# Kernel optimization log

Measured on AMD Instinct MI355X. Metric: run time of the kernel, lower is better.

The kernel has to match this reference:

```python
import jax, jax.numpy as jnp
import numpy as np

N = 50000   # nodes
E = 800000  # edges (avg degree 16)
IN, H, OUT = 128, 128, 128


def _lin(key, fan_in, fan_out):
    s = 1.0 / np.sqrt(fan_in)
    return jax.random.uniform(key, (fan_in, fan_out), minval=-s, maxval=s, dtype=jnp.float32)


def setup_inputs() -> dict:
    key = jax.random.key(0)
    ks = jax.random.split(key, 12)
    inp = {
        "x": jax.random.normal(ks[0], (N, IN), dtype=jnp.float32),
        "edge_index": jax.random.randint(ks[1], (2, E), 0, N, dtype=jnp.int64),
        # layer 1: in -> hidden
        "Wl1": _lin(ks[2], IN, H), "b1": jnp.zeros((H,), jnp.float32), "Wr1": _lin(ks[3], IN, H),
        # layer 2: hidden -> hidden
        "Wl2": _lin(ks[4], H, H), "b2": jnp.zeros((H,), jnp.float32), "Wr2": _lin(ks[5], H, H),
        # layer 3: hidden -> out
        "Wl3": _lin(ks[6], H, OUT), "b3": jnp.zeros((OUT,), jnp.float32), "Wr3": _lin(ks[7], H, OUT),
    }
    return inp


def _sage_conv(x, src, dst, inv_deg, Wl, b, Wr):
    # mean-aggregate neighbor messages: gather from src, scatter-sum to dst
    msg = jnp.take(x, src, axis=0)                       # [E, d]
    agg = jax.ops.segment_sum(msg, dst, num_segments=N)  # [N, d]
    mean = agg * inv_deg[:, None]                        # scatter-mean (0 for isolated)
    return mean @ Wl + b + x @ Wr


def reference(x, edge_index, Wl1, b1, Wr1, Wl2, b2, Wr2, Wl3, b3, Wr3):
    src, dst = edge_index[0], edge_index[1]
    deg = jax.ops.segment_sum(jnp.ones((E,), jnp.float32), dst, num_segments=N)
    inv_deg = jnp.where(deg > 0, 1.0 / jnp.maximum(deg, 1.0), 0.0)

    h = _sage_conv(x, src, dst, inv_deg, Wl1, b1, Wr1)
    h = jax.nn.relu(h)  # dropout p=0.5 is identity in eval mode
    h = _sage_conv(h, src, dst, inv_deg, Wl2, b2, Wr2)
    h = jax.nn.relu(h)
    h = _sage_conv(h, src, dst, inv_deg, Wl3, b3, Wr3)
    return h
```

## Files before the change

kernel.cpp:

```cpp
#include <hip/hip_runtime.h>


#define D 128

typedef __attribute__((ext_vector_type(8))) short bf16x8;
typedef __attribute__((ext_vector_type(4))) float f32x4;

__device__ inline ushort f2bf(float f) {
  union { float f; unsigned u; } v; v.f = f;
  unsigned r = v.u + 0x7fffu + ((v.u >> 16) & 1u);
  return (ushort)(r >> 16);
}
__device__ inline float bf2f(ushort h) {
  union { unsigned u; float f; } v; v.u = ((unsigned)h) << 16;
  return v.f;
}

__global__ __launch_bounds__(256) void k_bhist(const int* __restrict__ dst,
                                               int* __restrict__ bhist, int E, int NB) {
  __shared__ int h[512];
  int t = threadIdx.x;
  for (int i = t; i < NB; i += 256) h[i] = 0;
  __syncthreads();
  int beg = blockIdx.x * 4096;
  int end = min(beg + 4096, E);
  for (int i = beg + t; i < end; i += 256) atomicAdd(&h[dst[i] >> 7], 1);
  __syncthreads();
  for (int i = t; i < NB; i += 256)
    if (h[i]) atomicAdd(&bhist[i], h[i]);
}

__global__ __launch_bounds__(512) void k_bscan(const int* __restrict__ bhist,
                                               int* __restrict__ bbase,
                                               int* __restrict__ bcur,
                                               int* __restrict__ offN, int NB) {
  __shared__ int part[512];
  int t = threadIdx.x;
  part[t] = (t < NB) ? bhist[t] : 0;
  __syncthreads();
  for (int d = 1; d < 512; d <<= 1) {
    int x = part[t];
    int a = (t >= d) ? part[t - d] : 0;
    __syncthreads();
    part[t] = x + a;
    __syncthreads();
  }
  if (t < NB) {
    int b = (t == 0) ? 0 : part[t - 1];
    bbase[t] = b;
    bcur[t] = b;
  }
  if (t == NB - 1) *offN = part[t];
}

__global__ __launch_bounds__(256) void k_bucket(const int* __restrict__ src,
                                                const int* __restrict__ dst,
                                                int* __restrict__ bcur,
                                                unsigned* __restrict__ ebuf,
                                                int E, int NB) {
  __shared__ int h[512];
  __shared__ int base[512];
  int t = threadIdx.x;
  for (int i = t; i < NB; i += 256) h[i] = 0;
  __syncthreads();
  int beg = blockIdx.x * 4096;
  int end = min(beg + 4096, E);
  for (int i = beg + t; i < end; i += 256) atomicAdd(&h[dst[i] >> 7], 1);
  __syncthreads();
  for (int i = t; i < NB; i += 256) {
    int c = h[i];
    base[i] = c ? atomicAdd(&bcur[i], c) : 0;
    h[i] = 0;
  }
  __syncthreads();
  for (int i = beg + t; i < end; i += 256) {
    int d = dst[i];
    int b = d >> 7;
    int r = atomicAdd(&h[b], 1);
    ebuf[base[b] + r] = (((unsigned)src[i]) << 16) | (unsigned)d;
  }
}

__global__ __launch_bounds__(256) void k_csr(const unsigned* __restrict__ ebuf,
                                             const int* __restrict__ bbase,
                                             const int* __restrict__ bhist,
                                             int* __restrict__ off,
                                             float* __restrict__ invd,
                                             int* __restrict__ srcs, int N) {
  __shared__ int dcount[128];
  __shared__ int dloc[128];
  int b = blockIdx.x;
  int t = threadIdx.x;
  int beg = bbase[b];
  int end = beg + bhist[b];
  if (t < 128) dcount[t] = 0;
  __syncthreads();
  for (int i = beg + t; i < end; i += 256) atomicAdd(&dcount[ebuf[i] & 127], 1);
  __syncthreads();
  if (t < 128) dloc[t] = dcount[t];
  __syncthreads();
  for (int d = 1; d < 128; d <<= 1) {
    int x = 0, a = 0;
    if (t < 128) {
      x = dloc[t];
      if (t >= d) a = dloc[t - d];
    }
    __syncthreads();
    if (t < 128) dloc[t] = x + a;
    __syncthreads();
  }
  if (t < 128) {
    int node = b * 128 + t;
    if (node < N) {
      int ex = beg + dloc[t] - dcount[t];
      off[node] = ex;
      int c = dcount[t];
      invd[node] = c > 0 ? 1.0f / (float)c : 0.0f;
      dcount[t] = ex;
    }
  }
  __syncthreads();
  for (int i = beg + t; i < end; i += 256) {
    unsigned p = ebuf[i];
    int slot = atomicAdd(&dcount[p & 127], 1);
    srcs[slot] = (int)(p >> 16);
  }
}

__global__ void k_cast(const float* __restrict__ x, ushort* __restrict__ xb, int total4) {
  int i = blockIdx.x * blockDim.x + threadIdx.x;
  if (i >= total4) return;
  float4 v = *reinterpret_cast<const float4*>(x + (size_t)i * 4);
  ushort4 o;
  o.x = f2bf(v.x); o.y = f2bf(v.y); o.z = f2bf(v.z); o.w = f2bf(v.w);
  *reinterpret_cast<ushort4*>(xb + (size_t)i * 4) = o;
}

__global__ void k_pack3(const float* __restrict__ Wl1, const float* __restrict__ Wr1,
                        const float* __restrict__ Wl2, const float* __restrict__ Wr2,
                        const float* __restrict__ Wl3, const float* __restrict__ Wr3,
                        ushort* __restrict__ Bp) {
  int gidx = blockIdx.x * blockDim.x + threadIdx.x;
  int layer = gidx >> 15;
  int idx = gidx & 32767;
  const float* Wl = (layer == 0) ? Wl1 : (layer == 1) ? Wl2 : Wl3;
  const float* Wr = (layer == 0) ? Wr1 : (layer == 1) ? Wr2 : Wr3;
  int kk = idx >> 12;
  int ct = (idx >> 9) & 7;
  int l  = (idx >> 3) & 63;
  int j  = idx & 7;
  int k = kk * 32 + ((l >> 4) << 3) + j;
  int col = ct * 16 + (l & 15);
  float v = (k < 128) ? Wl[k * 128 + col] : Wr[(k - 128) * 128 + col];
  Bp[gidx] = f2bf(v);
}

template <int RELU, int FINAL>
__global__ __launch_bounds__(256, 6) void k_fused(const ushort* __restrict__ hin,
                                                  const int* __restrict__ off,
                                                  const int* __restrict__ srcs,
                                                  const float* __restrict__ invd,
                                                  const ushort* __restrict__ Bpack,
                                                  const float* __restrict__ bias,
                                                  float* __restrict__ outf,
                                                  ushort* __restrict__ outh, int N) {
  __shared__ ushort smean[16 * D];
  int t = threadIdx.x;
  int w = t >> 6;
  int lane = t & 63;
  int node0 = blockIdx.x * 16;
  int g = lane >> 4;
  int s = lane & 15;

  for (int q = 0; q < 4; ++q) {
    int nl = w * 4 + q;
    int n = node0 + nl;
    float acc[8] = {0.f, 0.f, 0.f, 0.f, 0.f, 0.f, 0.f, 0.f};
    float wgt = 0.f;
    if (n < N) {
      wgt = invd[n];
      int lo = off[n], hi = off[n + 1];
      int e = lo + g;
      for (; e + 4 < hi; e += 8) {
        int i0 = srcs[e];
        int i1 = srcs[e + 4];
        bf16x8 v0 = *reinterpret_cast<const bf16x8*>(hin + (size_t)i0 * D + s * 8);
        bf16x8 v1 = *reinterpret_cast<const bf16x8*>(hin + (size_t)i1 * D + s * 8);
#pragma unroll
        for (int j = 0; j < 8; ++j) acc[j] += bf2f((ushort)v0[j]);
#pragma unroll
        for (int j = 0; j < 8; ++j) acc[j] += bf2f((ushort)v1[j]);
      }
      if (e < hi) {
        int i0 = srcs[e];
        bf16x8 v0 = *reinterpret_cast<const bf16x8*>(hin + (size_t)i0 * D + s * 8);
#pragma unroll
        for (int j = 0; j < 8; ++j) acc[j] += bf2f((ushort)v0[j]);
      }
    }
#pragma unroll
    for (int j = 0; j < 8; ++j) acc[j] += __shfl_xor(acc[j], 16);
#pragma unroll
    for (int j = 0; j < 8; ++j) acc[j] += __shfl_xor(acc[j], 32);
    if (lane < 16) {
      bf16x8 o;
#pragma unroll
      for (int j = 0; j < 8; ++j) o[j] = (short)f2bf(acc[j] * wgt);
      int byte = nl * 256 + ((s * 16) ^ ((nl & 7) << 4));
      *reinterpret_cast<bf16x8*>(reinterpret_cast<char*>(smean) + byte) = o;
    }
  }
  __syncthreads();

  int lr = lane & 15;
  int kgrp = lane >> 4;
  int arow = node0 + lr;
  if (arow >= N) arow = N - 1;
  size_t abase = (size_t)arow * D;

  f32x4 acc2[2];
#pragma unroll
  for (int i = 0; i < 2; ++i) {
    float bv = bias[(w * 2 + i) * 16 + lr];
    acc2[i] = (f32x4){bv, bv, bv, bv};
  }

#pragma unroll
  for (int kk = 0; kk < 8; ++kk) {
    int klocal = ((kk & 3) << 5) + (kgrp << 3);
    bf16x8 a;
    if (kk < 4) {
      int byte = lr * 256 + ((klocal * 2) ^ ((lr & 7) << 4));
      a = *reinterpret_cast<const bf16x8*>(reinterpret_cast<const char*>(smean) + byte);
    } else {
      a = *reinterpret_cast<const bf16x8*>(hin + abase + klocal);
    }
#pragma unroll
    for (int i = 0; i < 2; ++i) {
      int ct = w * 2 + i;
      bf16x8 b = *reinterpret_cast<const bf16x8*>(Bpack + (((size_t)(kk * 8 + ct) * 64 + lane) << 3));
      acc2[i] = __builtin_amdgcn_mfma_f32_16x16x32_bf16(a, b, acc2[i], 0, 0, 0);
    }
  }

#pragma unroll
  for (int i = 0; i < 2; ++i) {
    int c = (w * 2 + i) * 16 + lr;
#pragma unroll
    for (int r = 0; r < 4; ++r) {
      int rr = node0 + kgrp * 4 + r;
      if (rr < N) {
        float v = acc2[i][r];
        if (RELU) v = fmaxf(v, 0.f);
        if (FINAL) outf[(size_t)rr * D + c] = v;
        else outh[(size_t)rr * D + c] = f2bf(v);
      }
    }
  }
}

extern "C" void kernel_launch(void* const* d_in, const int* in_sizes, int n_in,
                              void* d_out, int out_size, void* d_ws, size_t ws_size,
                              hipStream_t stream) {
  const float* x   = (const float*)d_in[0];
  const int*   ei  = (const int*)d_in[1];
  const float* Wl1 = (const float*)d_in[2];
  const float* b1  = (const float*)d_in[3];
  const float* Wr1 = (const float*)d_in[4];
  const float* Wl2 = (const float*)d_in[5];
  const float* b2  = (const float*)d_in[6];
  const float* Wr2 = (const float*)d_in[7];
  const float* Wl3 = (const float*)d_in[8];
  const float* b3  = (const float*)d_in[9];
  const float* Wr3 = (const float*)d_in[10];
  float* out = (float*)d_out;

  int N = in_sizes[0] / D;
  int E = in_sizes[1] / 2;
  const int* srcp = ei;
  const int* dstp = ei + E;
  int NB = (N + 127) >> 7;

  char* p = (char*)d_ws;
  auto carve = [&](size_t bytes) {
    void* r = (void*)p;
    p += (bytes + 255) & ~(size_t)255;
    return r;
  };
  int*      bhist = (int*)carve((size_t)512 * 4);
  int*      bbase = (int*)carve((size_t)512 * 4);
  int*      bcur  = (int*)carve((size_t)512 * 4);
  int*      off   = (int*)carve((size_t)(N + 1) * 4);
  float*    invd  = (float*)carve((size_t)N * 4);
  int*      srcs  = (int*)carve((size_t)E * 4);
  unsigned* ebuf  = (unsigned*)carve((size_t)E * 4);
  ushort*   xb    = (ushort*)carve((size_t)N * D * 2);
  ushort*   h1b   = (ushort*)carve((size_t)N * D * 2);
  ushort*   h2b   = (ushort*)carve((size_t)N * D * 2);
  ushort*   Bp    = (ushort*)carve((size_t)3 * 32768 * 2);

  hipMemsetAsync(bhist, 0, (size_t)NB * 4, stream);
  int ch_blocks = (E + 4095) / 4096;
  k_bhist<<<ch_blocks, 256, 0, stream>>>(dstp, bhist, E, NB);
  k_bscan<<<1, 512, 0, stream>>>(bhist, bbase, bcur, off + N, NB);
  k_bucket<<<ch_blocks, 256, 0, stream>>>(srcp, dstp, bcur, ebuf, E, NB);
  k_csr<<<NB, 256, 0, stream>>>(ebuf, bbase, bhist, off, invd, srcs, N);

  int total4 = N * D / 4;
  k_cast<<<(total4 + 255) / 256, 256, 0, stream>>>(x, xb, total4);
  k_pack3<<<3 * 32768 / 256, 256, 0, stream>>>(Wl1, Wr1, Wl2, Wr2, Wl3, Wr3, Bp);

  int fused_blocks = (N + 15) / 16;

  k_fused<1, 0><<<fused_blocks, 256, 0, stream>>>(xb, off, srcs, invd, Bp, b1, nullptr, h1b, N);
  k_fused<1, 0><<<fused_blocks, 256, 0, stream>>>(h1b, off, srcs, invd, Bp + 32768, b2, nullptr, h2b, N);
  k_fused<0, 1><<<fused_blocks, 256, 0, stream>>>(h2b, off, srcs, invd, Bp + 2 * 32768, b3, out, nullptr, N);
}
```

Measured before the change: 180.6 us.

## Fold bucket scan into histogram kernel and interleave two-node gathers

Removes the separate single-block scan launch: the last histogram block, found with an atomic counter in an unused slot of bhist (index 480), does a wavefront shuffle scan. The aggregation loop in the fused SAGE kernel now processes two nodes at once, issuing four independent row gathers per iteration so more memory loads are in flight. This trades one kernel launch and gather latency for higher register pressure and a dependence on NB staying below 480.

```diff
diff --git a/kernel.cpp b/kernel.cpp
--- a/kernel.cpp
+++ b/kernel.cpp
@@ -17,8 +17,13 @@
 }
 
 __global__ __launch_bounds__(256) void k_bhist(const int* __restrict__ dst,
-                                               int* __restrict__ bhist, int E, int NB) {
+                                               int* __restrict__ bhist,
+                                               int* __restrict__ bbase,
+                                               int* __restrict__ bcur,
+                                               int* __restrict__ offN,
+                                               int E, int NB, int nblocks) {
   __shared__ int h[512];
+  __shared__ int lastflag;
   int t = threadIdx.x;
   for (int i = t; i < NB; i += 256) h[i] = 0;
   __syncthreads();
@@ -28,29 +33,32 @@
   __syncthreads();
   for (int i = t; i < NB; i += 256)
     if (h[i]) atomicAdd(&bhist[i], h[i]);
-}
-
-__global__ __launch_bounds__(512) void k_bscan(const int* __restrict__ bhist,
-                                               int* __restrict__ bbase,
-                                               int* __restrict__ bcur,
-                                               int* __restrict__ offN, int NB) {
-  __shared__ int part[512];
-  int t = threadIdx.x;
-  part[t] = (t < NB) ? bhist[t] : 0;
-  __syncthreads();
-  for (int d = 1; d < 512; d <<= 1) {
-    int x = part[t];
-    int a = (t >= d) ? part[t - d] : 0;
-    __syncthreads();
-    part[t] = x + a;
-    __syncthreads();
-  }
-  if (t < NB) {
-    int b = (t == 0) ? 0 : part[t - 1];
-    bbase[t] = b;
-    bcur[t] = b;
-  }
-  if (t == NB - 1) *offN = part[t];
+  __threadfence();
+  if (t == 0) lastflag = (atomicAdd(&bhist[480], 1) == nblocks - 1);
+  __syncthreads();
+  if (!lastflag) return;
+  __threadfence();
+  if (t < 64) {
+    int lane = t;
+    int run = 0;
+    for (int base = 0; base < NB; base += 64) {
+      int idx = base + lane;
+      int orig = (idx < NB) ? bhist[idx] : 0;
+      int v = orig;
+#pragma unroll
+      for (int d = 1; d < 64; d <<= 1) {
+        int u = __shfl_up(v, d);
+        if (lane >= d) v += u;
+      }
+      if (idx < NB) {
+        int ex = run + v - orig;
+        bbase[idx] = ex;
+        bcur[idx] = ex;
+      }
+      run += __shfl(v, 63);
+    }
+    if (lane == 0) *offN = run;
+  }
 }
 
 __global__ __launch_bounds__(256) void k_bucket(const int* __restrict__ src,
@@ -172,42 +180,92 @@
   int g = lane >> 4;
   int s = lane & 15;
 
-  for (int q = 0; q < 4; ++q) {
-    int nl = w * 4 + q;
-    int n = node0 + nl;
-    float acc[8] = {0.f, 0.f, 0.f, 0.f, 0.f, 0.f, 0.f, 0.f};
-    float wgt = 0.f;
-    if (n < N) {
-      wgt = invd[n];
-      int lo = off[n], hi = off[n + 1];
-      int e = lo + g;
-      for (; e + 4 < hi; e += 8) {
-        int i0 = srcs[e];
-        int i1 = srcs[e + 4];
-        bf16x8 v0 = *reinterpret_cast<const bf16x8*>(hin + (size_t)i0 * D + s * 8);
-        bf16x8 v1 = *reinterpret_cast<const bf16x8*>(hin + (size_t)i1 * D + s * 8);
-#pragma unroll
-        for (int j = 0; j < 8; ++j) acc[j] += bf2f((ushort)v0[j]);
-#pragma unroll
-        for (int j = 0; j < 8; ++j) acc[j] += bf2f((ushort)v1[j]);
+#pragma unroll
+  for (int pq = 0; pq < 2; ++pq) {
+    int nlA = w * 4 + pq * 2;
+    int nlB = nlA + 1;
+    int nA = node0 + nlA, nB = node0 + nlB;
+    float accA[8] = {0.f, 0.f, 0.f, 0.f, 0.f, 0.f, 0.f, 0.f};
+    float accB[8] = {0.f, 0.f, 0.f, 0.f, 0.f, 0.f, 0.f, 0.f};
+    float wgtA = 0.f, wgtB = 0.f;
+    int loA = 0, hiA = 0, loB = 0, hiB = 0;
+    if (nA < N) { wgtA = invd[nA]; loA = off[nA]; hiA = off[nA + 1]; }
+    if (nB < N) { wgtB = invd[nB]; loB = off[nB]; hiB = off[nB + 1]; }
+    int eA = loA + g, eB = loB + g;
+
+    while (eA + 4 < hiA && eB + 4 < hiB) {
+      int i0 = srcs[eA];
+      int i1 = srcs[eA + 4];
+      int i2 = srcs[eB];
+      int i3 = srcs[eB + 4];
+      bf16x8 v0 = *reinterpret_cast<const bf16x8*>(hin + (size_t)i0 * D + s * 8);
+      bf16x8 v1 = *reinterpret_cast<const bf16x8*>(hin + (size_t)i1 * D + s * 8);
+      bf16x8 v2 = *reinterpret_cast<const bf16x8*>(hin + (size_t)i2 * D + s * 8);
+      bf16x8 v3 = *reinterpret_cast<const bf16x8*>(hin + (size_t)i3 * D + s * 8);
+#pragma unroll
+      for (int j = 0; j < 8; ++j) accA[j] += bf2f((ushort)v0[j]);
+#pragma unroll
+      for (int j = 0; j < 8; ++j) accA[j] += bf2f((ushort)v1[j]);
+#pragma unroll
+      for (int j = 0; j < 8; ++j) accB[j] += bf2f((ushort)v2[j]);
+#pragma unroll
+      for (int j = 0; j < 8; ++j) accB[j] += bf2f((ushort)v3[j]);
+      eA += 8; eB += 8;
+    }
+    for (; eA + 4 < hiA; eA += 8) {
+      int i0 = srcs[eA];
+      int i1 = srcs[eA + 4];
+      bf16x8 v0 = *reinterpret_cast<const bf16x8*>(hin + (size_t)i0 * D + s * 8);
+      bf16x8 v1 = *reinterpret_cast<const bf16x8*>(hin + (size_t)i1 * D + s * 8);
+#pragma unroll
+      for (int j = 0; j < 8; ++j) accA[j] += bf2f((ushort)v0[j]);
+#pragma unroll
+      for (int j = 0; j < 8; ++j) accA[j] += bf2f((ushort)v1[j]);
+    }
+    if (eA < hiA) {
+      int i0 = srcs[eA];
+      bf16x8 v0 = *reinterpret_cast<const bf16x8*>(hin + (size_t)i0 * D + s * 8);
+#pragma unroll
+      for (int j = 0; j < 8; ++j) accA[j] += bf2f((ushort)v0[j]);
+    }
+    for (; eB + 4 < hiB; eB += 8) {
+      int i0 = srcs[eB];
+      int i1 = srcs[eB + 4];
+      bf16x8 v0 = *reinterpret_cast<const bf16x8*>(hin + (size_t)i0 * D + s * 8);
+      bf16x8 v1 = *reinterpret_cast<const bf16x8*>(hin + (size_t)i1 * D + s * 8);
+#pragma unroll
+      for (int j = 0; j < 8; ++j) accB[j] += bf2f((ushort)v0[j]);
+#pragma unroll
+      for (int j = 0; j < 8; ++j) accB[j] += bf2f((ushort)v1[j]);
+    }
+    if (eB < hiB) {
+      int i0 = srcs[eB];
+      bf16x8 v0 = *reinterpret_cast<const bf16x8*>(hin + (size_t)i0 * D + s * 8);
+#pragma unroll
+      for (int j = 0; j < 8; ++j) accB[j] += bf2f((ushort)v0[j]);
+    }
+
+#pragma unroll
+    for (int j = 0; j < 8; ++j) {
+      accA[j] += __shfl_xor(accA[j], 16);
+      accB[j] += __shfl_xor(accB[j], 16);
+    }
+#pragma unroll
+    for (int j = 0; j < 8; ++j) {
+      accA[j] += __shfl_xor(accA[j], 32);
+      accB[j] += __shfl_xor(accB[j], 32);
+    }
+    if (lane < 16) {
+      bf16x8 oA, oB;
+#pragma unroll
+      for (int j = 0; j < 8; ++j) {
+        oA[j] = (short)f2bf(accA[j] * wgtA);
+        oB[j] = (short)f2bf(accB[j] * wgtB);
       }
-      if (e < hi) {
-        int i0 = srcs[e];
-        bf16x8 v0 = *reinterpret_cast<const bf16x8*>(hin + (size_t)i0 * D + s * 8);
-#pragma unroll
-        for (int j = 0; j < 8; ++j) acc[j] += bf2f((ushort)v0[j]);
-      }
-    }
-#pragma unroll
-    for (int j = 0; j < 8; ++j) acc[j] += __shfl_xor(acc[j], 16);
-#pragma unroll
-    for (int j = 0; j < 8; ++j) acc[j] += __shfl_xor(acc[j], 32);
-    if (lane < 16) {
-      bf16x8 o;
-#pragma unroll
-      for (int j = 0; j < 8; ++j) o[j] = (short)f2bf(acc[j] * wgt);
-      int byte = nl * 256 + ((s * 16) ^ ((nl & 7) << 4));
-      *reinterpret_cast<bf16x8*>(reinterpret_cast<char*>(smean) + byte) = o;
+      int byteA = nlA * 256 + ((s * 16) ^ ((nlA & 7) << 4));
+      int byteB = nlB * 256 + ((s * 16) ^ ((nlB & 7) << 4));
+      *reinterpret_cast<bf16x8*>(reinterpret_cast<char*>(smean) + byteA) = oA;
+      *reinterpret_cast<bf16x8*>(reinterpret_cast<char*>(smean) + byteB) = oB;
     }
   }
   __syncthreads();
@@ -299,10 +357,9 @@
   ushort*   h2b   = (ushort*)carve((size_t)N * D * 2);
   ushort*   Bp    = (ushort*)carve((size_t)3 * 32768 * 2);
 
-  hipMemsetAsync(bhist, 0, (size_t)NB * 4, stream);
+  hipMemsetAsync(bhist, 0, (size_t)512 * 4, stream);
   int ch_blocks = (E + 4095) / 4096;
-  k_bhist<<<ch_blocks, 256, 0, stream>>>(dstp, bhist, E, NB);
-  k_bscan<<<1, 512, 0, stream>>>(bhist, bbase, bcur, off + N, NB);
+  k_bhist<<<ch_blocks, 256, 0, stream>>>(dstp, bhist, bbase, bcur, off + N, E, NB, ch_blocks);
   k_bucket<<<ch_blocks, 256, 0, stream>>>(srcp, dstp, bcur, ebuf, E, NB);
   k_csr<<<NB, 256, 0, stream>>>(ebuf, bbase, bhist, off, invd, srcs, N);
 
```

New measurement: 184.4 us. 2.1% more time.
